# Optimization experiments

Measured on AMD Instinct MI355X. Metric: run time of the kernel, lower is better.

The kernel has to match this reference:

```python
import jax, jax.numpy as jnp
import numpy as np

N = 8192
IN_F = 512
OUT_F = 512
ALPHA = 0.2  # leaky relu slope


def setup_inputs() -> dict:
    key = jax.random.key(0)
    k1, k2, k3, k4, k5 = jax.random.split(key, 5)
    inp = jax.random.normal(k1, (N, IN_F), dtype=jnp.float32)
    adj = jax.random.randint(k2, (N, N), 0, 2, dtype=jnp.int32)
    # linear1: [in, out] + bias
    W1 = jax.random.normal(k3, (IN_F, OUT_F), dtype=jnp.float32) * (1.0 / np.sqrt(IN_F))
    b1 = jnp.zeros((OUT_F,), dtype=jnp.float32)
    # linear2: maps 2*out -> 1; split into the two halves acting on h_i and h_j
    a = jax.random.normal(k4, (2 * OUT_F,), dtype=jnp.float32) * (1.0 / np.sqrt(2 * OUT_F))
    a1 = a[:OUT_F]
    a2 = a[OUT_F:]
    b2 = jnp.zeros((), dtype=jnp.float32)
    return {"inp": inp, "adj": adj, "W1": W1, "b1": b1, "a1": a1, "a2": a2, "b2": b2}


def reference(inp, adj, W1, b1, a1, a2, b2):
    h = inp @ W1 + b1  # [N, out]
    # linear2(cat(h_i, h_j)) == h_i@a1 + h_j@a2 + b2 -> avoids the N*N*2F tensor
    e = jax.nn.leaky_relu((h @ a1)[:, None] + (h @ a2)[None, :] + b2, ALPHA)  # [N, N]
    attention = jnp.where(adj > 0, e, jnp.float32(-1e12))
    attention = jax.nn.softmax(attention, axis=1)
    h_prime = attention @ h  # [N, out]
    return jax.nn.elu(h_prime)  # concat=True
```

## Files before the change

### kernel.cpp

```cpp
#include <hip/hip_runtime.h>
#include <hip/hip_bf16.h>
#include <stdint.h>

#define NR 8192
#define FD 512
#define BM 64
#define BKC 256

typedef __attribute__((ext_vector_type(8))) short s8v;
typedef __attribute__((ext_vector_type(4))) float f32x4;

static __device__ __forceinline__ short bf16_rtne(float x) {
    union { float f; uint32_t u; } v; v.f = x;
    uint32_t r = (v.u + 0x7FFFu + ((v.u >> 16) & 1u)) >> 16;
    return (short)r;
}
static __device__ __forceinline__ float bf16_to_f32(short s) {
    union { uint32_t u; float f; } v; v.u = ((uint32_t)(uint16_t)s) << 16;
    return v.f;
}

__global__ void k_prepack(const int* __restrict__ adj,
                          unsigned long long* __restrict__ bm) {
    const int lane = threadIdx.x & 63;
    const int wv   = threadIdx.x >> 6;
    const int gid  = blockIdx.x * 4 + wv;
    const int row  = gid >> 2;
    const int seg  = (gid & 3) * 2048;
    const int* p   = adj + (size_t)row * NR + seg + lane;
    unsigned long long* o = bm + (((size_t)row * NR + seg) >> 6);
#pragma unroll
    for (int g = 0; g < 8; ++g) {
        unsigned long long b0 = __ballot(p[g * 256]       != 0);
        unsigned long long b1 = __ballot(p[g * 256 + 64]  != 0);
        unsigned long long b2 = __ballot(p[g * 256 + 128] != 0);
        unsigned long long b3 = __ballot(p[g * 256 + 192] != 0);
        unsigned long long vs = (lane == 0) ? b0 : (lane == 1) ? b1
                              : (lane == 2) ? b2 : b3;
        if (lane < 4) o[g * 4 + lane] = vs;
    }
}

__global__ void k_convert(const float* __restrict__ in, short* __restrict__ out) {
    int i = blockIdx.x * blockDim.x + threadIdx.x;
    float4 v = ((const float4*)in)[i];
    short4 s;
    s.x = bf16_rtne(v.x); s.y = bf16_rtne(v.y);
    s.z = bf16_rtne(v.z); s.w = bf16_rtne(v.w);
    ((short4*)out)[i] = s;
}

__global__ void k_w1t(const float* __restrict__ W1, short* __restrict__ W1T) {
    int i = blockIdx.x * 256 + threadIdx.x;
    int k = i & 511, n = i >> 9;
    W1T[(size_t)n * 512 + k] = bf16_rtne(W1[(size_t)k * 512 + n]);
}

__launch_bounds__(256)
__global__ void k_gemm_h(const short* __restrict__ A,
                         const short* __restrict__ BT,
                         const float* __restrict__ b1,
                         short* __restrict__ H,
                         short* __restrict__ HT2)
{
    const int lane = threadIdx.x & 63;
    const int wn   = threadIdx.x >> 6;
    const int m    = lane & 15;
    const int q    = lane >> 4;
    const int r0   = blockIdx.x * 32;
    const int c0   = blockIdx.y * 128 + wn * 32;

    f32x4 acc[2][2] = {};
#pragma unroll 1
    for (int k0 = 0; k0 < 512; k0 += 32) {
        s8v a[2], b[2];
#pragma unroll
        for (int rt = 0; rt < 2; ++rt)
            a[rt] = *(const s8v*)(A + (size_t)(r0 + rt * 16 + m) * 512 + k0 + q * 8);
#pragma unroll
        for (int nt = 0; nt < 2; ++nt)
            b[nt] = *(const s8v*)(BT + (size_t)(c0 + nt * 16 + m) * 512 + k0 + q * 8);
#pragma unroll
        for (int rt = 0; rt < 2; ++rt)
#pragma unroll
            for (int nt = 0; nt < 2; ++nt)
                acc[rt][nt] = __builtin_amdgcn_mfma_f32_16x16x32_bf16(a[rt], b[nt], acc[rt][nt], 0, 0, 0);
    }
    float b1v[2];
#pragma unroll
    for (int nt = 0; nt < 2; ++nt) b1v[nt] = b1[c0 + nt * 16 + m];

#pragma unroll
    for (int rt = 0; rt < 2; ++rt)
#pragma unroll
        for (int nt = 0; nt < 2; ++nt) {
            int col = c0 + nt * 16 + m;
            short4 hp;
#pragma unroll
            for (int r = 0; r < 4; ++r) {
                int row = r0 + rt * 16 + q * 4 + r;
                short hv = bf16_rtne(acc[rt][nt][r] + b1v[nt]);
                H[(size_t)row * 512 + col] = hv;
                ((short*)&hp)[r] = hv;
            }
            *(short4*)(HT2 + (size_t)blockIdx.x * (512 * 32) + (size_t)col * 32 + rt * 16 + q * 4) = hp;
        }
}

__global__ void k_f1f2(const short* __restrict__ H, const float* __restrict__ a1,
                       const float* __restrict__ a2, const float* __restrict__ b2,
                       float* __restrict__ f1, float* __restrict__ f2s)
{
    const int lane = threadIdx.x & 63;
    const int row  = blockIdx.x * 4 + (threadIdx.x >> 6);
    s8v hv = *(const s8v*)(H + (size_t)row * 512 + lane * 8);
    float4 a1l = ((const float4*)(a1 + lane * 8))[0];
    float4 a1h = ((const float4*)(a1 + lane * 8))[1];
    float4 a2l = ((const float4*)(a2 + lane * 8))[0];
    float4 a2h = ((const float4*)(a2 + lane * 8))[1];
    float hf[8];
#pragma unroll
    for (int i = 0; i < 8; ++i) hf[i] = bf16_to_f32(hv[i]);
    float s1 = hf[0] * a1l.x + hf[1] * a1l.y + hf[2] * a1l.z + hf[3] * a1l.w
             + hf[4] * a1h.x + hf[5] * a1h.y + hf[6] * a1h.z + hf[7] * a1h.w;
    float s2 = hf[0] * a2l.x + hf[1] * a2l.y + hf[2] * a2l.z + hf[3] * a2l.w
             + hf[4] * a2h.x + hf[5] * a2h.y + hf[6] * a2h.z + hf[7] * a2h.w;
#pragma unroll
    for (int o = 32; o > 0; o >>= 1) {
        s1 += __shfl_xor(s1, o);
        s2 += __shfl_xor(s2, o);
    }
    if (lane == 0) {
        f1[row]  = s1;
        f2s[row] = s2 + b2[0];
    }
}

__launch_bounds__(1024, 4)
__global__ void k_attn(const uint32_t* __restrict__ bm,
                       const short* __restrict__ HT2,
                       const float* __restrict__ f1,
                       const float* __restrict__ f2s,
                       float* __restrict__ nump,
                       float* __restrict__ denomp)
{
    __shared__ __align__(16) short wt[2][BM * BKC];

    const int t    = threadIdx.x;
    const int lane = t & 63;
    const int w    = t >> 6;
    const int m    = lane & 15;
    const int q    = lane >> 4;

    const int js   = blockIdx.x & 3;
    const int band = blockIdx.x >> 2;
    const int r0   = band * BM;
    const int jb0  = js * 2048;

    const int prow = t >> 4;
    const int jg   = t & 15;

    const float f1v = f1[r0 + prow];
    const uint16_t* bmp = (const uint16_t*)bm + (((size_t)(r0 + prow) * NR + jb0) >> 4) + jg;
    const float*    f2p = f2s + jb0 + jg * 16;

    f32x4 acc[4][2] = {};
    float dsum = 0.f;

    uint32_t bits;
    float4 fv[4];

#define GAT_PHASE1(PN)                                                        \
    {                                                                         \
        s8v wv0, wv1;                                                         \
        _Pragma("unroll")                                                     \
        for (int jj = 0; jj < 8; ++jj) {                                      \
            float s_ = f1v + ((const float*)fv)[jj];                          \
            float e_ = __expf(fmaxf(s_, 0.2f * s_));                          \
            float x_ = ((bits >> jj) & 1u) ? e_ : 0.f;                        \
            dsum += x_;                                                       \
            wv0[jj] = bf16_rtne(x_);                                          \
        }                                                                     \
        _Pragma("unroll")                                                     \
        for (int jj = 0; jj < 8; ++jj) {                                      \
            float s_ = f1v + ((const float*)fv)[8 + jj];                      \
            float e_ = __expf(fmaxf(s_, 0.2f * s_));                          \
            float x_ = ((bits >> (8 + jj)) & 1u) ? e_ : 0.f;                  \
            dsum += x_;                                                       \
            wv1[jj] = bf16_rtne(x_);                                          \
        }                                                                     \
        const int sw = prow & 15;                                             \
        *(s8v*)&wt[PN][prow * BKC + (((2 * jg) ^ sw) << 3)]     = wv0;        \
        *(s8v*)&wt[PN][prow * BKC + (((2 * jg + 1) ^ sw) << 3)] = wv1;        \
    }

    bits = bmp[0];
#pragma unroll
    for (int g = 0; g < 4; ++g) fv[g] = ((const float4*)f2p)[g];
    GAT_PHASE1(0)
    __syncthreads();

#pragma unroll 1
    for (int ch = 0; ch < 2048 / BKC; ++ch) {
        const int p   = ch & 1;
        const int chn = ch + 1;
        const bool more = (chn < 2048 / BKC);
        if (more) {
            bits = bmp[chn * 16];
#pragma unroll
            for (int g = 0; g < 4; ++g) fv[g] = ((const float4*)(f2p + chn * BKC))[g];
        }

#pragma unroll
        for (int kk = 0; kk < 8; ++kk) {
            const int jt = (jb0 + ch * BKC + kk * 32) >> 5;
            const short* hb = HT2 + (size_t)jt * 16384 + q * 8;
            s8v b0 = *(const s8v*)(hb + (size_t)(w * 32 + m) * 32);
            s8v b1 = *(const s8v*)(hb + (size_t)(w * 32 + 16 + m) * 32);
            s8v af[4];
#pragma unroll
            for (int i = 0; i < 4; ++i)
                af[i] = *(const s8v*)&wt[p][(i * 16 + m) * BKC + (((kk * 4 + q) ^ m) << 3)];
#pragma unroll
            for (int i = 0; i < 4; ++i) {
                acc[i][0] = __builtin_amdgcn_mfma_f32_16x16x32_bf16(af[i], b0, acc[i][0], 0, 0, 0);
                acc[i][1] = __builtin_amdgcn_mfma_f32_16x16x32_bf16(af[i], b1, acc[i][1], 0, 0, 0);
            }
        }

        if (more) GAT_PHASE1(p ^ 1)

        __syncthreads();
    }
#undef GAT_PHASE1

    dsum += __shfl_xor(dsum, 1);
    dsum += __shfl_xor(dsum, 2);
    dsum += __shfl_xor(dsum, 4);
    dsum += __shfl_xor(dsum, 8);
    if (jg == 0) denomp[(size_t)js * NR + r0 + prow] = dsum;

    float* np = nump + (size_t)js * NR * FD;
#pragma unroll
    for (int i = 0; i < 4; ++i)
#pragma unroll
        for (int nt = 0; nt < 2; ++nt)
#pragma unroll
            for (int r = 0; r < 4; ++r) {
                int row = r0 + i * 16 + q * 4 + r;
                int col = w * 32 + nt * 16 + m;
                np[(size_t)row * FD + col] = acc[i][nt][r];
            }
}

__global__ void k_combine(const float* __restrict__ nump,
                          const float* __restrict__ denomp,
                          float* __restrict__ out)
{
    size_t e = ((size_t)blockIdx.x * 256 + threadIdx.x) * 4;
    int row = (int)(e >> 9);
    float4 n0 = *(const float4*)(nump + e);
    float4 n1 = *(const float4*)(nump + (size_t)NR * FD + e);
    float4 n2 = *(const float4*)(nump + (size_t)2 * NR * FD + e);
    float4 n3 = *(const float4*)(nump + (size_t)3 * NR * FD + e);
    float d = denomp[row] + denomp[NR + row] + denomp[2 * NR + row] + denomp[3 * NR + row];
    float inv = 1.0f / d;
    float4 o;
    o.x = (n0.x + n1.x + n2.x + n3.x) * inv;
    o.y = (n0.y + n1.y + n2.y + n3.y) * inv;
    o.z = (n0.z + n1.z + n2.z + n3.z) * inv;
    o.w = (n0.w + n1.w + n2.w + n3.w) * inv;
    o.x = (o.x > 0.f) ? o.x : (__expf(o.x) - 1.f);
    o.y = (o.y > 0.f) ? o.y : (__expf(o.y) - 1.f);
    o.z = (o.z > 0.f) ? o.z : (__expf(o.z) - 1.f);
    o.w = (o.w > 0.f) ? o.w : (__expf(o.w) - 1.f);
    *(float4*)(out + e) = o;
}

extern "C" void kernel_launch(void* const* d_in, const int* in_sizes, int n_in,
                              void* d_out, int out_size, void* d_ws, size_t ws_size,
                              hipStream_t stream) {
    const float* inp = (const float*)d_in[0];
    const int*   adj = (const int*)d_in[1];
    const float* W1  = (const float*)d_in[2];
    const float* b1  = (const float*)d_in[3];
    const float* a1  = (const float*)d_in[4];
    const float* a2  = (const float*)d_in[5];
    const float* b2  = (const float*)d_in[6];
    float* out = (float*)d_out;

    short*    inp_bf = (short*)d_ws;
    short*    w1t    = inp_bf + (size_t)NR * FD;
    short*    h      = w1t + (size_t)FD * FD;
    short*    ht2    = h + (size_t)NR * FD;
    uint32_t* bmw    = (uint32_t*)(ht2 + (size_t)FD * NR);
    float*    f1     = (float*)(bmw + (size_t)NR * 256);
    float*    f2s    = f1 + NR;
    float*    nump   = f2s + NR;
    float*    denomp = nump + (size_t)4 * NR * FD;

    k_prepack<<<NR, 256, 0, stream>>>(adj, (unsigned long long*)bmw);
    k_convert<<<(NR * FD / 4) / 256, 256, 0, stream>>>(inp, inp_bf);
    k_w1t<<<(FD * FD) / 256, 256, 0, stream>>>(W1, w1t);
    dim3 g1(NR / 32, FD / 128);
    k_gemm_h<<<g1, 256, 0, stream>>>(inp_bf, w1t, b1, h, ht2);
    k_f1f2<<<NR / 4, 256, 0, stream>>>(h, a1, a2, b2, f1, f2s);
    k_attn<<<128 * 4, 1024, 0, stream>>>(bmw, ht2, f1, f2s, nump, denomp);
    k_combine<<<(NR * FD / 4) / 256, 256, 0, stream>>>(nump, denomp, out);
}
```

Measured before the change: 537.7 us.

## Stage H tiles into LDS via async global_load_lds with padded layout in attention kernel

The attention kernel now copies each 32-column slice of the transposed H matrix into double-buffered shared memory using direct global-to-LDS loads. The producer GEMM writes that slice with a padded stride of 36 so the LDS reads avoid bank conflicts. Blocks shrink to 512 threads, each wave covers 64 output columns instead of 32, and attention weights are generated per 32-wide chunk instead of per 256. The aim is to cut redundant global reads of H and overlap the copy of the next tile with the MFMA work, at the cost of one extra barrier per 32-column step and a larger workspace.

Measured after the change: 525.8 us. 1.02x faster.

```diff
diff --git a/kernel.cpp b/kernel.cpp
--- a/kernel.cpp
+++ b/kernel.cpp
@@ -5,7 +5,7 @@
 #define NR 8192
 #define FD 512
 #define BM 64
-#define BKC 256
+#define PADC 36
 
 typedef __attribute__((ext_vector_type(8))) short s8v;
 typedef __attribute__((ext_vector_type(4))) float f32x4;
@@ -61,7 +61,7 @@
                          const short* __restrict__ BT,
                          const float* __restrict__ b1,
                          short* __restrict__ H,
-                         short* __restrict__ HT2)
+                         short* __restrict__ HT36)
 {
     const int lane = threadIdx.x & 63;
     const int wn   = threadIdx.x >> 6;
@@ -103,7 +103,8 @@
                 H[(size_t)row * 512 + col] = hv;
                 ((short*)&hp)[r] = hv;
             }
-            *(short4*)(HT2 + (size_t)blockIdx.x * (512 * 32) + (size_t)col * 32 + rt * 16 + q * 4) = hp;
+            *(short4*)(HT36 + (size_t)blockIdx.x * (512 * PADC)
+                             + (size_t)col * PADC + rt * 16 + q * 4) = hp;
         }
 }
 
@@ -136,15 +137,16 @@
     }
 }
 
-__launch_bounds__(1024, 4)
+__launch_bounds__(512, 4)
 __global__ void k_attn(const uint32_t* __restrict__ bm,
-                       const short* __restrict__ HT2,
+                       const short* __restrict__ HT36,
                        const float* __restrict__ f1,
                        const float* __restrict__ f2s,
                        float* __restrict__ nump,
                        float* __restrict__ denomp)
 {
-    __shared__ __align__(16) short wt[2][BM * BKC];
+    __shared__ __align__(16) short bbuf[2][512 * PADC];
+    __shared__ __align__(16) short wt[2][BM * 32];
 
     const int t    = threadIdx.x;
     const int lane = t & 63;
@@ -157,98 +159,99 @@
     const int r0   = band * BM;
     const int jb0  = js * 2048;
 
-    const int prow = t >> 4;
-    const int jg   = t & 15;
+    const int prow = t >> 3;
+    const int jg   = t & 7;
 
     const float f1v = f1[r0 + prow];
-    const uint16_t* bmp = (const uint16_t*)bm + (((size_t)(r0 + prow) * NR + jb0) >> 4) + jg;
-    const float*    f2p = f2s + jb0 + jg * 16;
-
-    f32x4 acc[4][2] = {};
+    const uint32_t* bmrow = bm + (size_t)(r0 + prow) * 256 + js * 64;
+    const float*    f2p   = f2s + jb0 + jg * 4;
+
+    f32x4 acc[4][4] = {};
     float dsum = 0.f;
 
-    uint32_t bits;
-    float4 fv[4];
-
-#define GAT_PHASE1(PN)                                                        \
-    {                                                                         \
-        s8v wv0, wv1;                                                         \
-        _Pragma("unroll")                                                     \
-        for (int jj = 0; jj < 8; ++jj) {                                      \
-            float s_ = f1v + ((const float*)fv)[jj];                          \
-            float e_ = __expf(fmaxf(s_, 0.2f * s_));                          \
-            float x_ = ((bits >> jj) & 1u) ? e_ : 0.f;                        \
-            dsum += x_;                                                       \
-            wv0[jj] = bf16_rtne(x_);                                          \
-        }                                                                     \
-        _Pragma("unroll")                                                     \
-        for (int jj = 0; jj < 8; ++jj) {                                      \
-            float s_ = f1v + ((const float*)fv)[8 + jj];                      \
-            float e_ = __expf(fmaxf(s_, 0.2f * s_));                          \
-            float x_ = ((bits >> (8 + jj)) & 1u) ? e_ : 0.f;                  \
-            dsum += x_;                                                       \
-            wv1[jj] = bf16_rtne(x_);                                          \
-        }                                                                     \
-        const int sw = prow & 15;                                             \
-        *(s8v*)&wt[PN][prow * BKC + (((2 * jg) ^ sw) << 3)]     = wv0;        \
-        *(s8v*)&wt[PN][prow * BKC + (((2 * jg + 1) ^ sw) << 3)] = wv1;        \
-    }
-
-    bits = bmp[0];
-#pragma unroll
-    for (int g = 0; g < 4; ++g) fv[g] = ((const float4*)f2p)[g];
-    GAT_PHASE1(0)
+#define GAT_DMA(KT, PN)                                                        \
+    {                                                                          \
+        const short* srcb = HT36 + (size_t)(js * 64 + (KT)) * (512 * PADC);    \
+        short* dstb = &bbuf[PN][0];                                            \
+        _Pragma("unroll")                                                      \
+        for (int r_ = 0; r_ < 5; ++r_) {                                       \
+            int g_ = w + 8 * r_;                                               \
+            if (g_ < 36) {                                                     \
+                __builtin_amdgcn_global_load_lds(                              \
+                    (const __attribute__((address_space(1))) int*)             \
+                        (srcb + g_ * 512 + lane * 8),                          \
+                    (__attribute__((address_space(3))) int*)(dstb + g_ * 512), \
+                    16, 0, 0);                                                 \
+            }                                                                  \
+        }                                                                      \
+    }
+
+#define GAT_WGEN(KT, PN)                                                       \
+    {                                                                          \
+        uint32_t wd_ = bmrow[KT];                                              \
+        float4 f2_ = *(const float4*)(f2p + (KT) * 32);                        \
+        uint32_t nib_ = wd_ >> (jg * 4);                                       \
+        short4 sv_;                                                            \
+        _Pragma("unroll")                                                      \
+        for (int jj = 0; jj < 4; ++jj) {                                       \
+            float s_ = f1v + ((const float*)&f2_)[jj];                         \
+            float e_ = __expf(fmaxf(s_, 0.2f * s_));                           \
+            float x_ = ((nib_ >> jj) & 1u) ? e_ : 0.f;                         \
+            dsum += x_;                                                        \
+            ((short*)&sv_)[jj] = bf16_rtne(x_);                                \
+        }                                                                      \
+        *(short4*)&wt[PN][prow * 32 + (((jg >> 1) ^ (prow & 3)) << 3)          \
+                          + (jg & 1) * 4] = sv_;                               \
+    }
+
+    GAT_DMA(0, 0)
+    GAT_WGEN(0, 0)
     __syncthreads();
 
 #pragma unroll 1
-    for (int ch = 0; ch < 2048 / BKC; ++ch) {
-        const int p   = ch & 1;
-        const int chn = ch + 1;
-        const bool more = (chn < 2048 / BKC);
-        if (more) {
-            bits = bmp[chn * 16];
-#pragma unroll
-            for (int g = 0; g < 4; ++g) fv[g] = ((const float4*)(f2p + chn * BKC))[g];
+    for (int kk = 0; kk < 64; ++kk) {
+        const int p = kk & 1;
+        const bool more = (kk < 63);
+
+        if (more) GAT_DMA(kk + 1, p ^ 1)
+
+        s8v af[4];
+#pragma unroll
+        for (int i = 0; i < 4; ++i)
+            af[i] = *(const s8v*)&wt[p][(i * 16 + m) * 32 + ((q ^ (m & 3)) << 3)];
+        const short* bb = &bbuf[p][0];
+#pragma unroll
+        for (int nt = 0; nt < 4; ++nt) {
+            int col = w * 64 + nt * 16 + m;
+            union { short4 h[2]; s8v v; } bu;
+            bu.h[0] = *(const short4*)&bb[col * PADC + q * 8];
+            bu.h[1] = *(const short4*)&bb[col * PADC + q * 8 + 4];
+#pragma unroll
+            for (int i = 0; i < 4; ++i)
+                acc[i][nt] = __builtin_amdgcn_mfma_f32_16x16x32_bf16(af[i], bu.v, acc[i][nt], 0, 0, 0);
         }
 
-#pragma unroll
-        for (int kk = 0; kk < 8; ++kk) {
-            const int jt = (jb0 + ch * BKC + kk * 32) >> 5;
-            const short* hb = HT2 + (size_t)jt * 16384 + q * 8;
-            s8v b0 = *(const s8v*)(hb + (size_t)(w * 32 + m) * 32);
-            s8v b1 = *(const s8v*)(hb + (size_t)(w * 32 + 16 + m) * 32);
-            s8v af[4];
-#pragma unroll
-            for (int i = 0; i < 4; ++i)
-                af[i] = *(const s8v*)&wt[p][(i * 16 + m) * BKC + (((kk * 4 + q) ^ m) << 3)];
-#pragma unroll
-            for (int i = 0; i < 4; ++i) {
-                acc[i][0] = __builtin_amdgcn_mfma_f32_16x16x32_bf16(af[i], b0, acc[i][0], 0, 0, 0);
-                acc[i][1] = __builtin_amdgcn_mfma_f32_16x16x32_bf16(af[i], b1, acc[i][1], 0, 0, 0);
-            }
-        }
-
-        if (more) GAT_PHASE1(p ^ 1)
+        if (more) GAT_WGEN(kk + 1, p ^ 1)
 
         __syncthreads();
     }
-#undef GAT_PHASE1
+#undef GAT_DMA
+#undef GAT_WGEN
 
     dsum += __shfl_xor(dsum, 1);
     dsum += __shfl_xor(dsum, 2);
     dsum += __shfl_xor(dsum, 4);
-    dsum += __shfl_xor(dsum, 8);
     if (jg == 0) denomp[(size_t)js * NR + r0 + prow] = dsum;
 
     float* np = nump + (size_t)js * NR * FD;
 #pragma unroll
     for (int i = 0; i < 4; ++i)
 #pragma unroll
-        for (int nt = 0; nt < 2; ++nt)
+        for (int nt = 0; nt < 4; ++nt)
 #pragma unroll
             for (int r = 0; r < 4; ++r) {
                 int row = r0 + i * 16 + q * 4 + r;
-                int col = w * 32 + nt * 16 + m;
+                int col = w * 64 + nt * 16 + m;
                 np[(size_t)row * FD + col] = acc[i][nt][r];
             }
 }
@@ -292,8 +295,8 @@
     short*    inp_bf = (short*)d_ws;
     short*    w1t    = inp_bf + (size_t)NR * FD;
     short*    h      = w1t + (size_t)FD * FD;
-    short*    ht2    = h + (size_t)NR * FD;
-    uint32_t* bmw    = (uint32_t*)(ht2 + (size_t)FD * NR);
+    short*    ht36   = h + (size_t)NR * FD;
+    uint32_t* bmw    = (uint32_t*)(ht36 + (size_t)256 * 512 * PADC);
     float*    f1     = (float*)(bmw + (size_t)NR * 256);
     float*    f2s    = f1 + NR;
     float*    nump   = f2s + NR;
@@ -303,8 +306,8 @@
     k_convert<<<(NR * FD / 4) / 256, 256, 0, stream>>>(inp, inp_bf);
     k_w1t<<<(FD * FD) / 256, 256, 0, stream>>>(W1, w1t);
     dim3 g1(NR / 32, FD / 128);
-    k_gemm_h<<<g1, 256, 0, stream>>>(inp_bf, w1t, b1, h, ht2);
+    k_gemm_h<<<g1, 256, 0, stream>>>(inp_bf, w1t, b1, h, ht36);
     k_f1f2<<<NR / 4, 256, 0, stream>>>(h, a1, a2, b2, f1, f2s);
-    k_attn<<<128 * 4, 1024, 0, stream>>>(bmw, ht2, f1, f2s, nump, denomp);
+    k_attn<<<128 * 4, 512, 0, stream>>>(bmw, ht36, f1, f2s, nump, denomp);
     k_combine<<<(NR * FD / 4) / 256, 256, 0, stream>>>(nump, denomp, out);
 }
```
